# Kernel tuning notes

Measured on AMD Instinct MI355X. Metric: run time of the kernel, lower is better.

The kernel has to match this reference:

```python
import jax, jax.numpy as jnp
import numpy as np

EPS = 1e-5

def layer_norm(x, g, b):
    mu = jnp.mean(x, axis=-1, keepdims=True)
    var = jnp.var(x, axis=-1, keepdims=True)
    return (x - mu) * jax.lax.rsqrt(var + EPS) * g + b

def setup_inputs() -> dict:
    key = jax.random.key(0)
    N, C, K = 50000, 64, 16
    ks = jax.random.split(key, 16)
    def lin(k, fan_in, fan_out):
        bound = 1.0 / np.sqrt(fan_in)
        kw, kb = jax.random.split(k)
        W = jax.random.uniform(kw, (fan_in, fan_out), minval=-bound, maxval=bound, dtype=jnp.float32)
        b = jax.random.uniform(kb, (fan_out,), minval=-bound, maxval=bound, dtype=jnp.float32)
        return W, b
    wq, bq = lin(ks[0], C, C)
    wk, bk = lin(ks[1], C, C)
    wv, bv = lin(ks[2], C, C)
    wp, bp = lin(ks[3], 3, C)
    wg1, bg1 = lin(ks[4], C, C)
    wg2, bg2 = lin(ks[5], C, C)
    wo, bo = lin(ks[6], C, C)
    return {
        'points': jax.random.normal(ks[7], (N, 3), dtype=jnp.float32),
        'features': jax.random.normal(ks[8], (N, C), dtype=jnp.float32),
        'neighbor_idx': jax.random.randint(ks[9], (N, K), 0, N, dtype=jnp.int32),
        'wq': wq, 'bq': bq, 'wk': wk, 'bk': bk, 'wv': wv, 'bv': bv,
        'wp': wp, 'bp': bp, 'gp': jnp.ones((C,), jnp.float32), 'betap': jnp.zeros((C,), jnp.float32),
        'wg1': wg1, 'bg1': bg1, 'gg': jnp.ones((C,), jnp.float32), 'betag': jnp.zeros((C,), jnp.float32),
        'wg2': wg2, 'bg2': bg2, 'wo': wo, 'bo': bo,
    }

def reference(points, features, neighbor_idx, wq, bq, wk, bk, wv, bv,
              wp, bp, gp, betap, wg1, bg1, gg, betag, wg2, bg2, wo, bo):
    # residual_proj is Identity since in_planes == out_planes
    residual = features
    q = features @ wq + bq                      # (N, C)
    k = features @ wk + bk
    v = features @ wv + bv
    gpts = points[neighbor_idx]                 # (N, K, 3)
    gk = k[neighbor_idx]                        # (N, K, C)
    gv = v[neighbor_idx]
    rel = gpts - points[:, None, :]             # (N, K, 3)
    p = jax.nn.relu(layer_norm(rel @ wp + bp, gp, betap))  # (N, K, C)
    attn_in = q[:, None, :] - gk + p            # (N, K, C)
    h = jax.nn.relu(layer_norm(attn_in @ wg1 + bg1, gg, betag))
    w = h @ wg2 + bg2                           # (N, K, C)
    w = jax.nn.softmax(w, axis=1)               # softmax over neighbor axis
    out = jnp.sum((gv + p) * w, axis=1)         # (N, C)
    return out @ wo + bo + residual
```

## Files before the change

### kernel.cpp

```cpp
#include <hip/hip_runtime.h>

typedef __attribute__((ext_vector_type(8))) short bfrag8;
typedef __attribute__((ext_vector_type(4))) short bfrag4;
typedef __attribute__((ext_vector_type(4))) float f32x4;
typedef __attribute__((ext_vector_type(4))) int   i32x4;

__device__ __forceinline__ float bf2f(unsigned short h){
  unsigned u = ((unsigned)h) << 16;
  return __builtin_bit_cast(float, u);
}
__device__ __forceinline__ unsigned short f2bf(float f){
  unsigned u = __builtin_bit_cast(unsigned, f);
  u = u + 0x7FFFu + ((u >> 16) & 1u);
  return (unsigned short)(u >> 16);
}
__device__ __forceinline__ bfrag8 gload8(const unsigned short* p){
  int4 v = *(const int4*)p;
  return __builtin_bit_cast(bfrag8, v);
}
__device__ __forceinline__ bfrag8 neg8(bfrag8 x){
  i32x4 u = __builtin_bit_cast(i32x4, x);
#pragma unroll
  for (int i = 0; i < 4; i++) u[i] ^= 0x80008000;
  return __builtin_bit_cast(bfrag8, u);
}
__device__ __forceinline__ bfrag8 lds_load8(const unsigned short* p){
  bfrag4 lo = *(const bfrag4*)p;
  bfrag4 hi = *(const bfrag4*)(p + 4);
  bfrag8 r;
#pragma unroll
  for (int j = 0; j < 4; j++){ r[j] = lo[j]; r[4+j] = hi[j]; }
  return r;
}
__device__ __forceinline__ f32x4 mfma16(bfrag8 a, bfrag8 b, f32x4 c){
  return __builtin_amdgcn_mfma_f32_16x16x32_bf16(a, b, c, 0, 0, 0);
}

__device__ __forceinline__ float ldf(const void* p, size_t i, int f32){
  return f32 ? ((const float*)p)[i] : bf2f(((const unsigned short*)p)[i]);
}
__device__ __forceinline__ unsigned short ldbf(const void* p, size_t i, int f32){
  return f32 ? f2bf(((const float*)p)[i]) : ((const unsigned short*)p)[i];
}
__device__ __forceinline__ bfrag8 load8bf(const void* p, size_t base, int f32){
  if (f32){
    const float* f = (const float*)p + base;
    float4 x = *(const float4*)f;
    float4 y = *(const float4*)(f + 4);
    bfrag8 r;
    r[0]=(short)f2bf(x.x); r[1]=(short)f2bf(x.y); r[2]=(short)f2bf(x.z); r[3]=(short)f2bf(x.w);
    r[4]=(short)f2bf(y.x); r[5]=(short)f2bf(y.y); r[6]=(short)f2bf(y.z); r[7]=(short)f2bf(y.w);
    return r;
  }
  return gload8((const unsigned short*)p + base);
}

template<int CTRL>
__device__ __forceinline__ float dpp_add(float x){
  int xi = __builtin_bit_cast(int, x);
  int yi = __builtin_amdgcn_update_dpp(0, xi, CTRL, 0xF, 0xF, true);
  return x + __builtin_bit_cast(float, yi);
}
__device__ __forceinline__ float row16_sum(float x){
  x = dpp_add<0xB1>(x);
  x = dpp_add<0x4E>(x);
  x = dpp_add<0x141>(x);
  x = dpp_add<0x140>(x);
  return x;
}
__device__ __forceinline__ float xgrp_sum(float x){
  x += __shfl_xor(x, 16, 64);
  x += __shfl_xor(x, 32, 64);
  return x;
}
__device__ __forceinline__ float xgrp_max(float x){
  x = fmaxf(x, __shfl_xor(x, 16, 64));
  x = fmaxf(x, __shfl_xor(x, 32, 64));
  return x;
}

struct Ptrs { const void* p[21]; int n[21]; };
struct PrepPtrs { const void* w[6]; const void* wp; const void* b[11]; };

__device__ int classify_f32(const unsigned short* p, int n){
  int m = n < 128 ? n : 128;
  int insane = 0, evenZero = 0, evenCnt = 0, oddNZ = 0, oddCnt = 0;
  for (int i = 0; i < m; i++){
    unsigned short h = p[i];
    int e = (h >> 7) & 0xFF;
    bool z = (h & 0x7FFF) == 0;
    if (!z && (e == 0xFF || e < 90 || e > 140)) insane++;
    if (i & 1){ oddCnt++;  if (!z) oddNZ++; }
    else      { evenCnt++; if (z)  evenZero++; }
  }
  if (insane > 0) return 1;
  if (evenZero * 4 >= evenCnt * 3 && oddNZ * 4 >= oddCnt * 3) return 1;
  return 0;
}

__global__ void detect_kernel(Ptrs ptrs, int* flags){
  int t = threadIdx.x;
  if (t >= 21) return;
  flags[t] = (t == 2) ? 0 : classify_f32((const unsigned short*)ptrs.p[t], ptrs.n[t]);
}

__global__ void prep_kernel(PrepPtrs pp, const int* __restrict__ flags,
                            unsigned short* __restrict__ wfrag,
                            unsigned short* __restrict__ wp_bf,
                            float* __restrict__ biases)
{
  const int gid = blockIdx.x * 256 + threadIdx.x;
  const int gstride = gridDim.x * 256;
  const int wflag[6] = {3,5,7,13,17,19};
  for (int idx = gid; idx < 6*4096; idx += gstride){
    int m = idx >> 12;
    int r = idx & 4095;
    int j = r & 7;
    int lane = (r >> 3) & 63;
    int kt = r >> 9;
    int ks = kt >> 2, t = kt & 3;
    int o = lane >> 4, rl = lane & 15;
    int src = (ks*32 + o*8 + j)*64 + t*16 + rl;
    wfrag[idx] = ldbf(pp.w[m], src, flags[wflag[m]]);
  }
  if (blockIdx.x == 0){
    for (int i = threadIdx.x; i < 192; i += 256) wp_bf[i] = ldbf(pp.wp, i, flags[9]);
    const int bflag[11] = {4,6,8,10,11,12,14,15,16,18,20};
    for (int i = threadIdx.x; i < 11*64; i += 256){
      int m = i >> 6;
      biases[i] = ldf(pp.b[m], i & 63, flags[bflag[m]]);
    }
  }
}

__global__ __launch_bounds__(256, 2)
void qkv_kernel(const void* __restrict__ feat,
                const unsigned short* __restrict__ wfrag,
                const float* __restrict__ biases,
                unsigned short* __restrict__ q_ws, unsigned short* __restrict__ k_ws,
                unsigned short* __restrict__ v_ws, const int* __restrict__ flags, int N)
{
  const int F_feat = flags[1];
  const int lane = threadIdx.x & 63;
  const int wave = threadIdx.x >> 6;
  const int o = lane >> 4, rl = lane & 15;

  bfrag8 wqf[2][4], wkf[2][4], wvf[2][4];
#pragma unroll
  for (int ks = 0; ks < 2; ks++)
#pragma unroll
    for (int t = 0; t < 4; t++){
      int off = ((ks*4 + t)*64 + lane)*8;
      wqf[ks][t] = gload8(wfrag + off);
      wkf[ks][t] = gload8(wfrag + 4096 + off);
      wvf[ks][t] = gload8(wfrag + 8192 + off);
    }
  float bqC[4], bkC[4], bvC[4];
#pragma unroll
  for (int t = 0; t < 4; t++){
    bqC[t] = biases[0*64 + t*16 + rl];
    bkC[t] = biases[1*64 + t*16 + rl];
    bvC[t] = biases[2*64 + t*16 + rl];
  }

  const int ntiles = (N + 15) >> 4;
  for (int tile = blockIdx.x*4 + wave; tile < ntiles; tile += gridDim.x*4){
    const int n0 = tile * 16;
    int ar = n0 + rl; if (ar >= N) ar = N - 1;
    bfrag8 a[2];
#pragma unroll
    for (int ks = 0; ks < 2; ks++) a[ks] = load8bf(feat, (size_t)ar*64 + ks*32 + o*8, F_feat);

#pragma unroll
    for (int t = 0; t < 4; t++){
      f32x4 zq = {0.f,0.f,0.f,0.f}, zk = {0.f,0.f,0.f,0.f}, zv = {0.f,0.f,0.f,0.f};
#pragma unroll
      for (int ks = 0; ks < 2; ks++){
        zq = mfma16(a[ks], wqf[ks][t], zq);
        zk = mfma16(a[ks], wkf[ks][t], zk);
        zv = mfma16(a[ks], wvf[ks][t], zv);
      }
#pragma unroll
      for (int q = 0; q < 4; q++){
        size_t row = n0 + o*4 + q; int col = t*16 + rl;
        if ((int)row < N){
          q_ws[row*64 + col] = f2bf(zq[q] + bqC[t]);
          k_ws[row*64 + col] = f2bf(zk[q] + bkC[t]);
          v_ws[row*64 + col] = f2bf(zv[q] + bvC[t]);
        }
      }
    }
  }
}

__global__ __launch_bounds__(256, 2)
void pt_kernel(const void* __restrict__ points,
               const void* __restrict__ feat,
               const int* __restrict__ nidx,
               const unsigned short* __restrict__ q_ws,
               const unsigned short* __restrict__ k_ws,
               const unsigned short* __restrict__ v_ws,
               const unsigned short* __restrict__ wfrag,
               const unsigned short* __restrict__ wp_bf,
               const float* __restrict__ biases,
               const int* __restrict__ flags, void* __restrict__ out, int N)
{
  __shared__ unsigned short xbuf[4][16][68];
  __shared__ unsigned short ybuf[4][64];

  const int F_pts = flags[0], F_feat = flags[1];
  const int lane = threadIdx.x & 63;
  const int wave = threadIdx.x >> 6;
  const int o = lane >> 4, rl = lane & 15;

  bfrag8 wg1f[2][4], wg2f[2][4], wof[2][4];
#pragma unroll
  for (int ks = 0; ks < 2; ks++)
#pragma unroll
    for (int t = 0; t < 4; t++){
      int off = ((ks*4 + t)*64 + lane)*8;
      wg1f[ks][t] = gload8(wfrag + 3*4096 + off);
      wg2f[ks][t] = gload8(wfrag + 4*4096 + off);
      wof[ks][t]  = gload8(wfrag + 5*4096 + off);
    }
  bfrag8 wpf[4];
#pragma unroll
  for (int t = 0; t < 4; t++){
    bfrag8 a = {0,0,0,0,0,0,0,0};
    if (o == 0){
#pragma unroll
      for (int j = 0; j < 3; j++) a[j] = (short)wp_bf[j*64 + t*16 + rl];
    }
    wpf[t] = a;
  }
  float bpC[4], gpC[4], bePC[4], bg1C[4], ggC[4], beGC[4], bg2C[4], boC[4];
#pragma unroll
  for (int t = 0; t < 4; t++){
    int c = t*16 + rl;
    bpC[t]  = biases[3*64 + c];  gpC[t]  = biases[4*64 + c];  bePC[t] = biases[5*64 + c];
    bg1C[t] = biases[6*64 + c];  ggC[t]  = biases[7*64 + c];  beGC[t] = biases[8*64 + c];
    bg2C[t] = biases[9*64 + c];  boC[t]  = biases[10*64 + c];
  }

  const int wstride = gridDim.x * 4;
  for (int n = blockIdx.x*4 + wave; n < N; n += wstride){
    const int jr = nidx[n*16 + rl];
    int jq[4];
#pragma unroll
    for (int q = 0; q < 4; q++) jq[q] = nidx[n*16 + o*4 + q];

    unsigned short gvu[4][4];
#pragma unroll
    for (int q = 0; q < 4; q++)
#pragma unroll
      for (int t = 0; t < 4; t++) gvu[q][t] = v_ws[(size_t)jq[q]*64 + t*16 + rl];
    const float res = ldf(feat, (size_t)n*64 + lane, F_feat);
    float rel[3];
#pragma unroll
    for (int d = 0; d < 3; d++)
      rel[d] = ldf(points, (size_t)jr*3 + d, F_pts) - ldf(points, (size_t)n*3 + d, F_pts);
    bfrag8 qv[2], gkn[2];
#pragma unroll
    for (int ks = 0; ks < 2; ks++){
      qv[ks]  = gload8(q_ws + (size_t)n*64  + ks*32 + o*8);
      gkn[ks] = neg8(gload8(k_ws + (size_t)jr*64 + ks*32 + o*8));
    }

    bfrag8 ap = {0,0,0,0,0,0,0,0};
    if (o == 0){
#pragma unroll
      for (int d = 0; d < 3; d++) ap[d] = (short)f2bf(rel[d]);
    }
    f32x4 pacc[4];
#pragma unroll
    for (int t = 0; t < 4; t++){
      f32x4 z = {0.f,0.f,0.f,0.f};
      pacc[t] = mfma16(ap, wpf[t], z);
    }
    float p_val[4][4];
#pragma unroll
    for (int q = 0; q < 4; q++){
      float xv[4]; float s = 0.f, s2 = 0.f;
#pragma unroll
      for (int t = 0; t < 4; t++){ xv[t] = pacc[t][q] + bpC[t]; s += xv[t]; s2 += xv[t]*xv[t]; }
      s = row16_sum(s); s2 = row16_sum(s2);
      float mu = s * (1.f/64.f);
      float var = s2 * (1.f/64.f) - mu*mu;
      float rs = rsqrtf(var + 1e-5f);
#pragma unroll
      for (int t = 0; t < 4; t++){
        float v = (xv[t] - mu) * rs * gpC[t] + bePC[t];
        p_val[t][q] = fmaxf(v, 0.f);
      }
    }

#pragma unroll
    for (int q = 0; q < 4; q++)
#pragma unroll
      for (int t = 0; t < 4; t++) xbuf[wave][o*4 + q][t*16 + rl] = f2bf(p_val[t][q]);
    f32x4 hacc[4] = {{0.f,0.f,0.f,0.f},{0.f,0.f,0.f,0.f},{0.f,0.f,0.f,0.f},{0.f,0.f,0.f,0.f}};
#pragma unroll
    for (int ks = 0; ks < 2; ks++){
      bfrag8 pA = lds_load8(&xbuf[wave][rl][ks*32 + o*8]);
#pragma unroll
      for (int t = 0; t < 4; t++){
        hacc[t] = mfma16(pA,      wg1f[ks][t], hacc[t]);
        hacc[t] = mfma16(qv[ks],  wg1f[ks][t], hacc[t]);
        hacc[t] = mfma16(gkn[ks], wg1f[ks][t], hacc[t]);
      }
    }

    float h_val[4][4];
#pragma unroll
    for (int q = 0; q < 4; q++){
      float xv[4]; float s = 0.f, s2 = 0.f;
#pragma unroll
      for (int t = 0; t < 4; t++){ xv[t] = hacc[t][q] + bg1C[t]; s += xv[t]; s2 += xv[t]*xv[t]; }
      s = row16_sum(s); s2 = row16_sum(s2);
      float mu = s * (1.f/64.f);
      float var = s2 * (1.f/64.f) - mu*mu;
      float rs = rsqrtf(var + 1e-5f);
#pragma unroll
      for (int t = 0; t < 4; t++){
        float v = (xv[t] - mu) * rs * ggC[t] + beGC[t];
        h_val[t][q] = fmaxf(v, 0.f);
      }
    }

#pragma unroll
    for (int q = 0; q < 4; q++)
#pragma unroll
      for (int t = 0; t < 4; t++) xbuf[wave][o*4 + q][t*16 + rl] = f2bf(h_val[t][q]);
    f32x4 wacc[4] = {{0.f,0.f,0.f,0.f},{0.f,0.f,0.f,0.f},{0.f,0.f,0.f,0.f},{0.f,0.f,0.f,0.f}};
#pragma unroll
    for (int ks = 0; ks < 2; ks++){
      bfrag8 hf = lds_load8(&xbuf[wave][rl][ks*32 + o*8]);
#pragma unroll
      for (int t = 0; t < 4; t++) wacc[t] = mfma16(hf, wg2f[ks][t], wacc[t]);
    }

    float y[4];
#pragma unroll
    for (int t = 0; t < 4; t++){
      float wv[4];
#pragma unroll
      for (int q = 0; q < 4; q++) wv[q] = wacc[t][q] + bg2C[t];
      float mx = fmaxf(fmaxf(wv[0], wv[1]), fmaxf(wv[2], wv[3]));
      mx = xgrp_max(mx);
      float se = 0.f, z = 0.f;
#pragma unroll
      for (int q = 0; q < 4; q++){
        float e = __expf(wv[q] - mx);
        se += e;
        z  += e * (bf2f(gvu[q][t]) + p_val[t][q]);
      }
      se = xgrp_sum(se); z = xgrp_sum(z);
      y[t] = z / se;
    }

    if (o == 0){
#pragma unroll
      for (int t = 0; t < 4; t++) ybuf[wave][t*16 + rl] = f2bf(y[t]);
    }
    f32x4 oacc[4] = {{0.f,0.f,0.f,0.f},{0.f,0.f,0.f,0.f},{0.f,0.f,0.f,0.f},{0.f,0.f,0.f,0.f}};
#pragma unroll
    for (int ks = 0; ks < 2; ks++){
      bfrag8 yf = lds_load8(&ybuf[wave][ks*32 + o*8]);
#pragma unroll
      for (int t = 0; t < 4; t++) oacc[t] = mfma16(yf, wof[ks][t], oacc[t]);
    }

    float ov = 0.f;
#pragma unroll
    for (int t = 0; t < 4; t++) if (o == t) ov = oacc[t][0] + boC[t];
    float outv = ov + res;
    if (F_feat) ((float*)out)[(size_t)n*64 + lane] = outv;
    else ((unsigned short*)out)[(size_t)n*64 + lane] = f2bf(outv);
  }
}

extern "C" void kernel_launch(void* const* d_in, const int* in_sizes, int n_in,
                              void* d_out, int out_size, void* d_ws, size_t ws_size,
                              hipStream_t stream)
{
  const int N = in_sizes[1] / 64;

  unsigned short* q_ws = (unsigned short*)d_ws;
  unsigned short* k_ws = q_ws + (size_t)N * 64;
  unsigned short* v_ws = k_ws + (size_t)N * 64;
  char* base = (char*)d_ws + (size_t)3 * N * 64 * sizeof(unsigned short);
  int*            flags  = (int*)base;
  unsigned short* wfrag  = (unsigned short*)(base + 256);
  unsigned short* wp_bf  = (unsigned short*)(base + 256 + 49152);
  float*          biases = (float*)(base + 256 + 49152 + 512);

  Ptrs ptrs;
  for (int i = 0; i < 21; i++){ ptrs.p[i] = d_in[i]; ptrs.n[i] = in_sizes[i]; }
  PrepPtrs pp;
  pp.w[0] = d_in[3];  pp.w[1] = d_in[5];  pp.w[2] = d_in[7];
  pp.w[3] = d_in[13]; pp.w[4] = d_in[17]; pp.w[5] = d_in[19];
  pp.wp = d_in[9];
  pp.b[0] = d_in[4];  pp.b[1] = d_in[6];  pp.b[2] = d_in[8];  pp.b[3] = d_in[10];
  pp.b[4] = d_in[11]; pp.b[5] = d_in[12]; pp.b[6] = d_in[14]; pp.b[7] = d_in[15];
  pp.b[8] = d_in[16]; pp.b[9] = d_in[18]; pp.b[10] = d_in[20];

  detect_kernel<<<1, 64, 0, stream>>>(ptrs, flags);
  prep_kernel<<<32, 256, 0, stream>>>(pp, flags, wfrag, wp_bf, biases);
  qkv_kernel<<<512, 256, 0, stream>>>(d_in[1], wfrag, biases, q_ws, k_ws, v_ws, flags, N);
  pt_kernel<<<1024, 256, 0, stream>>>(d_in[0], d_in[1], (const int*)d_in[2], q_ws, k_ws, v_ws,
                                      wfrag, wp_bf, biases, flags, d_out, N);
}
```

Measured before the change: 238.4 us.

## Fuse q-gk+p before first gate matmul and parallelize dtype detection

The attention input q - gk + p is now formed in fp32 registers and written once to LDS as bf16. The first gate matmul then runs one MFMA per tile instead of three separate MFMAs for p, q and negated gk. To do this, gk is gathered element-wise per neighbor alongside gv rather than as fragment loads. Separately, the input-dtype detection kernel now uses one wave per tensor with shuffle reductions instead of a serial per-thread loop. The trade is a third fewer gate MFMAs for more scattered scalar gathers and extra registers.

```diff
diff --git a/kernel.cpp b/kernel.cpp
--- a/kernel.cpp
+++ b/kernel.cpp
@@ -3,7 +3,6 @@
 typedef __attribute__((ext_vector_type(8))) short bfrag8;
 typedef __attribute__((ext_vector_type(4))) short bfrag4;
 typedef __attribute__((ext_vector_type(4))) float f32x4;
-typedef __attribute__((ext_vector_type(4))) int   i32x4;
 
 __device__ __forceinline__ float bf2f(unsigned short h){
   unsigned u = ((unsigned)h) << 16;
@@ -17,12 +16,6 @@
 __device__ __forceinline__ bfrag8 gload8(const unsigned short* p){
   int4 v = *(const int4*)p;
   return __builtin_bit_cast(bfrag8, v);
-}
-__device__ __forceinline__ bfrag8 neg8(bfrag8 x){
-  i32x4 u = __builtin_bit_cast(i32x4, x);
-#pragma unroll
-  for (int i = 0; i < 4; i++) u[i] ^= 0x80008000;
-  return __builtin_bit_cast(bfrag8, u);
 }
 __device__ __forceinline__ bfrag8 lds_load8(const unsigned short* p){
   bfrag4 lo = *(const bfrag4*)p;
@@ -78,30 +71,45 @@
   x = fmaxf(x, __shfl_xor(x, 32, 64));
   return x;
 }
+__device__ __forceinline__ int wave_isum(int x){
+#pragma unroll
+  for (int s = 1; s < 64; s <<= 1) x += __shfl_xor(x, s, 64);
+  return x;
+}
 
 struct Ptrs { const void* p[21]; int n[21]; };
 struct PrepPtrs { const void* w[6]; const void* wp; const void* b[11]; };
 
-__device__ int classify_f32(const unsigned short* p, int n){
-  int m = n < 128 ? n : 128;
+__global__ void detect_kernel(Ptrs ptrs, int* flags){
+  const int lane = threadIdx.x & 63;
+  const int wid = blockIdx.x * 4 + (threadIdx.x >> 6);
+  if (wid >= 21) return;
+  if (wid == 2){ if (lane == 0) flags[2] = 0; return; }
+
+  const unsigned short* p = (const unsigned short*)ptrs.p[wid];
+  int m = ptrs.n[wid]; if (m > 128) m = 128;
   int insane = 0, evenZero = 0, evenCnt = 0, oddNZ = 0, oddCnt = 0;
-  for (int i = 0; i < m; i++){
-    unsigned short h = p[i];
-    int e = (h >> 7) & 0xFF;
-    bool z = (h & 0x7FFF) == 0;
-    if (!z && (e == 0xFF || e < 90 || e > 140)) insane++;
-    if (i & 1){ oddCnt++;  if (!z) oddNZ++; }
-    else      { evenCnt++; if (z)  evenZero++; }
-  }
-  if (insane > 0) return 1;
-  if (evenZero * 4 >= evenCnt * 3 && oddNZ * 4 >= oddCnt * 3) return 1;
-  return 0;
-}
-
-__global__ void detect_kernel(Ptrs ptrs, int* flags){
-  int t = threadIdx.x;
-  if (t >= 21) return;
-  flags[t] = (t == 2) ? 0 : classify_f32((const unsigned short*)ptrs.p[t], ptrs.n[t]);
+#pragma unroll
+  for (int s = 0; s < 2; s++){
+    int i = lane + s*64;
+    if (i < m){
+      unsigned short h = p[i];
+      int e = (h >> 7) & 0xFF;
+      bool z = (h & 0x7FFF) == 0;
+      if (!z && (e == 0xFF || e < 90 || e > 140)) insane++;
+      if (i & 1){ oddCnt++;  if (!z) oddNZ++; }
+      else      { evenCnt++; if (z)  evenZero++; }
+    }
+  }
+  insane = wave_isum(insane);
+  evenZero = wave_isum(evenZero); evenCnt = wave_isum(evenCnt);
+  oddNZ = wave_isum(oddNZ);       oddCnt = wave_isum(oddCnt);
+  if (lane == 0){
+    int f = 0;
+    if (insane > 0) f = 1;
+    else if (evenZero * 4 >= evenCnt * 3 && oddNZ * 4 >= oddCnt * 3) f = 1;
+    flags[wid] = f;
+  }
 }
 
 __global__ void prep_kernel(PrepPtrs pp, const int* __restrict__ flags,
@@ -249,22 +257,21 @@
 #pragma unroll
     for (int q = 0; q < 4; q++) jq[q] = nidx[n*16 + o*4 + q];
 
-    unsigned short gvu[4][4];
+    float qC[4], gkC[4][4], gvC[4][4];
+#pragma unroll
+    for (int t = 0; t < 4; t++) qC[t] = bf2f(q_ws[(size_t)n*64 + t*16 + rl]);
 #pragma unroll
     for (int q = 0; q < 4; q++)
 #pragma unroll
-      for (int t = 0; t < 4; t++) gvu[q][t] = v_ws[(size_t)jq[q]*64 + t*16 + rl];
+      for (int t = 0; t < 4; t++){
+        gkC[t][q] = bf2f(k_ws[(size_t)jq[q]*64 + t*16 + rl]);
+        gvC[t][q] = bf2f(v_ws[(size_t)jq[q]*64 + t*16 + rl]);
+      }
     const float res = ldf(feat, (size_t)n*64 + lane, F_feat);
     float rel[3];
 #pragma unroll
     for (int d = 0; d < 3; d++)
       rel[d] = ldf(points, (size_t)jr*3 + d, F_pts) - ldf(points, (size_t)n*3 + d, F_pts);
-    bfrag8 qv[2], gkn[2];
-#pragma unroll
-    for (int ks = 0; ks < 2; ks++){
-      qv[ks]  = gload8(q_ws + (size_t)n*64  + ks*32 + o*8);
-      gkn[ks] = neg8(gload8(k_ws + (size_t)jr*64 + ks*32 + o*8));
-    }
 
     bfrag8 ap = {0,0,0,0,0,0,0,0};
     if (o == 0){
@@ -297,17 +304,14 @@
 #pragma unroll
     for (int q = 0; q < 4; q++)
 #pragma unroll
-      for (int t = 0; t < 4; t++) xbuf[wave][o*4 + q][t*16 + rl] = f2bf(p_val[t][q]);
+      for (int t = 0; t < 4; t++)
+        xbuf[wave][o*4 + q][t*16 + rl] = f2bf(qC[t] - gkC[t][q] + p_val[t][q]);
     f32x4 hacc[4] = {{0.f,0.f,0.f,0.f},{0.f,0.f,0.f,0.f},{0.f,0.f,0.f,0.f},{0.f,0.f,0.f,0.f}};
 #pragma unroll
     for (int ks = 0; ks < 2; ks++){
-      bfrag8 pA = lds_load8(&xbuf[wave][rl][ks*32 + o*8]);
-#pragma unroll
-      for (int t = 0; t < 4; t++){
-        hacc[t] = mfma16(pA,      wg1f[ks][t], hacc[t]);
-        hacc[t] = mfma16(qv[ks],  wg1f[ks][t], hacc[t]);
-        hacc[t] = mfma16(gkn[ks], wg1f[ks][t], hacc[t]);
-      }
+      bfrag8 af = lds_load8(&xbuf[wave][rl][ks*32 + o*8]);
+#pragma unroll
+      for (int t = 0; t < 4; t++) hacc[t] = mfma16(af, wg1f[ks][t], hacc[t]);
     }
 
     float h_val[4][4];
@@ -352,7 +356,7 @@
       for (int q = 0; q < 4; q++){
         float e = __expf(wv[q] - mx);
         se += e;
-        z  += e * (bf2f(gvu[q][t]) + p_val[t][q]);
+        z  += e * (gvC[t][q] + p_val[t][q]);
       }
       se = xgrp_sum(se); z = xgrp_sum(z);
       y[t] = z / se;
@@ -404,7 +408,7 @@
   pp.b[4] = d_in[11]; pp.b[5] = d_in[12]; pp.b[6] = d_in[14]; pp.b[7] = d_in[15];
   pp.b[8] = d_in[16]; pp.b[9] = d_in[18]; pp.b[10] = d_in[20];
 
-  detect_kernel<<<1, 64, 0, stream>>>(ptrs, flags);
+  detect_kernel<<<6, 256, 0, stream>>>(ptrs, flags);
   prep_kernel<<<32, 256, 0, stream>>>(pp, flags, wfrag, wp_bf, biases);
   qkv_kernel<<<512, 256, 0, stream>>>(d_in[1], wfrag, biases, q_ws, k_ws, v_ws, flags, N);
   pt_kernel<<<1024, 256, 0, stream>>>(d_in[0], d_in[1], (const int*)d_in[2], q_ws, k_ws, v_ws,
```

New measurement: 224.9 us. -5.6%, faster.
